# Kernel tuning notes

Hardware: AMD Instinct MI355X
Metric: run time of the kernel (lower is better)

Reference implementation:

```python
import jax, jax.numpy as jnp
import numpy as np

OS_FACTOR = 1.5

def setup_inputs() -> dict:
    key = jax.random.key(0)
    k = jax.random.split(key, 5)
    B, T, I, H = 64, 1024, 1024, 1024
    s = 1.0 / np.sqrt(H).astype(np.float32)
    return {
        "x": jax.random.normal(k[0], (B, T, I), dtype=jnp.float32),
        "W_ih": jax.random.normal(k[1], (H, I), dtype=jnp.float32) * s,
        "W_hh": jax.random.normal(k[2], (H, H), dtype=jnp.float32) * s,
        "b_ih": jax.random.normal(k[3], (H,), dtype=jnp.float32) * s,
        "b_hh": jax.random.normal(k[4], (H,), dtype=jnp.float32) * s,
    }

def reference(x, W_ih, W_hh, b_ih, b_hh):
    B, T, I = x.shape
    H = W_hh.shape[0]
    delay_near = int(np.floor(OS_FACTOR))   # 1
    delay_far = int(np.ceil(OS_FACTOR))     # 2
    alpha = jnp.float32(OS_FACTOR - delay_near)  # 0.5
    # Precompute input projection for all steps (same math, batched GEMM): [T,B,H]
    xw = jnp.einsum('bti,hi->tbh', x, W_ih) + b_ih + b_hh
    # Circular delay buffer of the last `delay_far` states, zero-initialized.
    # In the torch code, negative indices into the zero `states` buffer read zeros,
    # which matches a zero-initialized buffer here.
    buf0 = jnp.zeros((delay_far, B, H), dtype=x.dtype)

    def step(buf, xw_t):
        # buf[-1] = state at t-1, buf[0] = state at t-delay_far
        h_read = (1.0 - alpha) * buf[delay_far - delay_near] + alpha * buf[0]
        h = jnp.tanh(xw_t + h_read @ W_hh.T)
        buf = jnp.concatenate([buf[1:], h[None]], axis=0)
        return buf, h

    _, states = jax.lax.scan(step, buf0, xw)   # states: [T,B,H]
    states = jnp.swapaxes(states, 0, 1)        # [B,T,H]
    h_final = states[:, -1, :][None]           # [1,B,H]
    return states, h_final
```

## Files before the change

### kernel.cpp

```cpp
#include <hip/hip_runtime.h>
#include <stdint.h>
#include <stddef.h>

#define TT 1024
#define BB 64
#define HH 1024
#define II 1024

typedef __attribute__((ext_vector_type(8))) short s16x8;
typedef __attribute__((ext_vector_type(4))) float f32x4;

#define WS_FLAGS 512
#define WS_RING  4096

static __device__ __forceinline__ unsigned short f2bf(float f) {
    union { float f; unsigned int u; } v; v.f = f;
    return (unsigned short)((v.u + 0x7fffu + ((v.u >> 16) & 1u)) >> 16);
}

static __device__ __forceinline__ s16x8 pack8(float4 a, float4 b) {
    s16x8 v;
    v[0] = (short)f2bf(a.x); v[1] = (short)f2bf(a.y);
    v[2] = (short)f2bf(a.z); v[3] = (short)f2bf(a.w);
    v[4] = (short)f2bf(b.x); v[5] = (short)f2bf(b.y);
    v[6] = (short)f2bf(b.z); v[7] = (short)f2bf(b.w);
    return v;
}

static __device__ __forceinline__ f32x4 zero4() {
    f32x4 v = {0.f, 0.f, 0.f, 0.f};
    return v;
}

static __device__ __forceinline__ s16x8 ld16_sc01(const void* p) {
    s16x8 v;
    asm volatile("global_load_dwordx4 %0, %1, off sc0 sc1" : "=v"(v) : "v"(p));
    return v;
}
static __device__ __forceinline__ void st_h(void* p, unsigned short val) {
    unsigned v32 = val;
    asm volatile("global_store_short %0, %1, off sc0 sc1" :: "v"(p), "v"(v32) : "memory");
}
#define WAITV(n) do { asm volatile("s_waitcnt vmcnt(" #n ")" ::: "memory"); \
                      __builtin_amdgcn_sched_barrier(0); } while (0)

__global__ void init_ws(unsigned int* w) {
    for (int i = threadIdx.x; i < 640; i += 256)
        __hip_atomic_store(&w[i], 0u, __ATOMIC_RELAXED, __HIP_MEMORY_SCOPE_AGENT);
}

__global__ __launch_bounds__(256, 2) void xw_gemm(
    const float* __restrict__ X,
    const float* __restrict__ Wih,
    const float* __restrict__ bih,
    const float* __restrict__ bhh,
    float* __restrict__ out)
{
    __shared__ unsigned short As[128 * 64];
    __shared__ unsigned short Bs[128 * 64];

    const int tid  = threadIdx.x;
    const int lane = tid & 63;
    const int wid  = tid >> 6;
    const int bm = blockIdx.x >> 3;
    const int bn = blockIdx.x & 7;
    const size_t m0 = (size_t)bm * 128;
    const int n0 = bn * 128;
    const int wm = (wid >> 1) * 64;
    const int wn = (wid & 1) * 64;

    f32x4 acc[4][4];
#pragma unroll
    for (int i = 0; i < 4; ++i)
#pragma unroll
        for (int jj = 0; jj < 4; ++jj) acc[i][jj] = zero4();

    const int srow  = tid >> 1;
    const int shalf = tid & 1;
    const float* xp = X   + (m0 + srow) * (size_t)II + shalf * 32;
    const float* wp = Wih + (size_t)(n0 + srow) * II + shalf * 32;

    for (int kt = 0; kt < II / 64; ++kt) {
#pragma unroll
        for (int i = 0; i < 4; ++i) {
            float4 a0 = *(const float4*)(xp + i * 8);
            float4 a1 = *(const float4*)(xp + i * 8 + 4);
            float4 b0 = *(const float4*)(wp + i * 8);
            float4 b1 = *(const float4*)(wp + i * 8 + 4);
            const int c = shalf * 4 + i;
            const int cw = (c ^ (srow & 7)) << 3;
            *(s16x8*)&As[srow * 64 + cw] = pack8(a0, a1);
            *(s16x8*)&Bs[srow * 64 + cw] = pack8(b0, b1);
        }
        __syncthreads();

#pragma unroll
        for (int kk = 0; kk < 2; ++kk) {
            s16x8 af[4], bf[4];
            const int cs = kk * 4 + (lane >> 4);
#pragma unroll
            for (int mi = 0; mi < 4; ++mi) {
                const int r = wm + mi * 16 + (lane & 15);
                af[mi] = *(const s16x8*)&As[r * 64 + ((cs ^ (r & 7)) << 3)];
            }
#pragma unroll
            for (int ni = 0; ni < 4; ++ni) {
                const int r = wn + ni * 16 + (lane & 15);
                bf[ni] = *(const s16x8*)&Bs[r * 64 + ((cs ^ (r & 7)) << 3)];
            }
#pragma unroll
            for (int mi = 0; mi < 4; ++mi)
#pragma unroll
                for (int ni = 0; ni < 4; ++ni)
                    acc[mi][ni] = __builtin_amdgcn_mfma_f32_16x16x32_bf16(
                        af[mi], bf[ni], acc[mi][ni], 0, 0, 0);
        }
        __syncthreads();
        xp += 64; wp += 64;
    }

#pragma unroll
    for (int ni = 0; ni < 4; ++ni) {
        const int col = n0 + wn + ni * 16 + (lane & 15);
        const float bias = bih[col] + bhh[col];
#pragma unroll
        for (int mi = 0; mi < 4; ++mi) {
            const size_t row = m0 + wm + mi * 16 + ((lane >> 4) << 2);
#pragma unroll
            for (int r = 0; r < 4; ++r)
                out[(row + r) * (size_t)HH + col] = acc[mi][ni][r] + bias;
        }
    }
}

__global__ __launch_bounds__(256, 1) void rnn_scan(
    const float* __restrict__ Whh,
    float* __restrict__ out,
    void* __restrict__ ws)
{
    __shared__ unsigned short Hl[16 * 1024];

    const int tid  = threadIdx.x;
    const int lane = tid & 63;
    const int wid  = tid >> 6;
    const int g  = blockIdx.x >> 4;
    const int sl = blockIdx.x & 15;

    const int j  = sl * 64 + wid * 16 + (lane & 15);
    const int kg = lane >> 4;

    s16x8 bfr[32];
    {
        const float* wr = Whh + (size_t)j * HH + kg * 8;
#pragma unroll
        for (int c = 0; c < 32; ++c) {
            float4 p0 = *(const float4*)(wr + c * 32);
            float4 p1 = *(const float4*)(wr + c * 32 + 4);
            bfr[c] = pack8(p0, p1);
        }
    }

    unsigned* fl = (unsigned*)((char*)ws + WS_FLAGS) + g * 64;
    char* rg = (char*)ws + WS_RING + (size_t)g * 65536;

    const int srow = tid >> 4;
    const int sseg = tid & 15;
    const char* sbase0 = rg + srow * 2048 + sseg * 16;
    const char* sbase1 = sbase0 + 32768;

    const int arow = lane & 15;
    const int brow = kg * 4;
    float hprev[4];

#pragma unroll
    for (int r = 0; r < 4; ++r) {
        const int b = g * 16 + brow + r;
        const size_t idx = ((size_t)b * TT) * HH + j;
        const float h = tanhf(out[idx]);
        out[idx] = h;
        hprev[r] = h;
        st_h(rg + 32768 + (brow + r) * 2048 + j * 2, f2bf(0.5f * h));
    }
    asm volatile("s_waitcnt vmcnt(0)" ::: "memory");
    __syncthreads();
    if (tid == 0)
        __hip_atomic_store(&fl[sl], 1u, __ATOMIC_RELAXED, __HIP_MEMORY_SCOPE_AGENT);

#pragma unroll 1
    for (int t = 1; t < TT; ++t) {
        float xwv[4]; size_t xidx[4];
#pragma unroll
        for (int r = 0; r < 4; ++r) {
            const int b = g * 16 + brow + r;
            xidx[r] = ((size_t)b * TT + t) * HH + j;
            xwv[r] = out[xidx[r]];
        }

        {
            const unsigned* myp = fl + (lane & 15);
            for (;;) {
                unsigned v = __hip_atomic_load(myp, __ATOMIC_RELAXED,
                                               __HIP_MEMORY_SCOPE_AGENT);
                if (__all((int)(v >= (unsigned)t))) break;
                __builtin_amdgcn_s_sleep(1);
            }
            asm volatile("" ::: "memory");
            __builtin_amdgcn_sched_barrier(0);
        }

        {
            const char* sp = (t & 1) ? sbase1 : sbase0;
            s16x8 v[8];
#pragma unroll
            for (int i = 0; i < 8; ++i) v[i] = ld16_sc01(sp + i * 256);
#pragma unroll
            for (int i = 0; i < 8; ++i) {
                if (i == 0)      { WAITV(7); }
                else if (i == 1) { WAITV(6); }
                else if (i == 2) { WAITV(5); }
                else if (i == 3) { WAITV(4); }
                else if (i == 4) { WAITV(3); }
                else if (i == 5) { WAITV(2); }
                else if (i == 6) { WAITV(1); }
                else             { WAITV(0); }
                const int c = sseg + i * 16;
                *(s16x8*)&Hl[srow * 1024 + ((c ^ (srow & 7)) << 3)] = v[i];
            }
        }
        __syncthreads();

        f32x4 acc[4];
#pragma unroll
        for (int i = 0; i < 4; ++i) acc[i] = zero4();
#pragma unroll
        for (int kb = 0; kb < 4; ++kb) {
            s16x8 a8[8];
#pragma unroll
            for (int ki = 0; ki < 8; ++ki) {
                const int cs = (kb * 8 + ki) * 4 + kg;
                a8[ki] = *(const s16x8*)&Hl[arow * 1024 + ((cs ^ (arow & 7)) << 3)];
            }
#pragma unroll
            for (int ki = 0; ki < 8; ++ki)
                acc[ki & 3] = __builtin_amdgcn_mfma_f32_16x16x32_bf16(
                    a8[ki], bfr[kb * 8 + ki], acc[ki & 3], 0, 0, 0);
        }
        f32x4 accT = acc[0] + acc[1] + acc[2] + acc[3];

        char* rw = rg + (size_t)((t + 1) & 1) * 32768;
#pragma unroll
        for (int r = 0; r < 4; ++r) {
            const float h = tanhf(accT[r] + xwv[r]);
            out[xidx[r]] = h;
            if (t == TT - 1)
                out[(size_t)BB * TT * HH +
                    (size_t)(g * 16 + brow + r) * HH + j] = h;
            else
                st_h(rw + (brow + r) * 2048 + j * 2, f2bf(0.5f * (h + hprev[r])));
            hprev[r] = h;
        }
        if (t < TT - 1) {
            asm volatile("s_waitcnt vmcnt(0)" ::: "memory");
            __syncthreads();
            if (tid == 0)
                __hip_atomic_store(&fl[sl], (unsigned)(t + 1),
                                   __ATOMIC_RELAXED, __HIP_MEMORY_SCOPE_AGENT);
        }
    }
}

extern "C" void kernel_launch(void* const* d_in, const int* in_sizes, int n_in,
                              void* d_out, int out_size, void* d_ws, size_t ws_size,
                              hipStream_t stream)
{
    const float* X   = (const float*)d_in[0];
    const float* Wih = (const float*)d_in[1];
    const float* Whh = (const float*)d_in[2];
    const float* bih = (const float*)d_in[3];
    const float* bhh = (const float*)d_in[4];
    float* out = (float*)d_out;

    init_ws<<<dim3(1), dim3(256), 0, stream>>>((unsigned int*)d_ws);
    xw_gemm<<<dim3(4096), dim3(256), 0, stream>>>(X, Wih, bih, bhh, out);
    rnn_scan<<<dim3(64), dim3(256), 0, stream>>>(Whh, out, d_ws);
}
```

Measured before the change: 3.811 ms.

## Halve scan blocks, transpose MFMA operands, and vectorize state stores

The recurrent scan now runs 32 blocks of 512 threads, 8 per batch group instead of 16, so each block owns 128 hidden units and waits on fewer peer flags. W_hh becomes the A operand of the MFMA so each lane's output holds 4 contiguous hidden units for one batch row. That allows float4 loads and stores of xw and h, and 8-byte packed bf16 ring stores in place of scalar shorts. Flag polling moves to a single wave that reads all 8 flags with two vector loads, followed by a block barrier. In exchange each block does more work per step and runs a larger barrier, and only 32 CUs are used.

Measured after the change: 4.488 ms. 17.8% more time.

```diff
diff --git a/kernel.cpp b/kernel.cpp
--- a/kernel.cpp
+++ b/kernel.cpp
@@ -9,6 +9,8 @@
 
 typedef __attribute__((ext_vector_type(8))) short s16x8;
 typedef __attribute__((ext_vector_type(4))) float f32x4;
+typedef __attribute__((ext_vector_type(4))) unsigned u32x4;
+typedef __attribute__((ext_vector_type(2))) unsigned u32x2;
 
 #define WS_FLAGS 512
 #define WS_RING  4096
@@ -37,9 +39,14 @@
     asm volatile("global_load_dwordx4 %0, %1, off sc0 sc1" : "=v"(v) : "v"(p));
     return v;
 }
-static __device__ __forceinline__ void st_h(void* p, unsigned short val) {
-    unsigned v32 = val;
-    asm volatile("global_store_short %0, %1, off sc0 sc1" :: "v"(p), "v"(v32) : "memory");
+static __device__ __forceinline__ u32x4 ld16u_wait(const void* p) {
+    u32x4 v;
+    asm volatile("global_load_dwordx4 %0, %1, off sc0 sc1\n\ts_waitcnt vmcnt(0)"
+                 : "=v"(v) : "v"(p) : "memory");
+    return v;
+}
+static __device__ __forceinline__ void st8_sc01(void* p, u32x2 v) {
+    asm volatile("global_store_dwordx2 %0, %1, off sc0 sc1" :: "v"(p), "v"(v) : "memory");
 }
 #define WAITV(n) do { asm volatile("s_waitcnt vmcnt(" #n ")" ::: "memory"); \
                       __builtin_amdgcn_sched_barrier(0); } while (0)
@@ -133,7 +140,7 @@
     }
 }
 
-__global__ __launch_bounds__(256, 1) void rnn_scan(
+__global__ __launch_bounds__(512, 1) void rnn_scan(
     const float* __restrict__ Whh,
     float* __restrict__ out,
     void* __restrict__ ws)
@@ -143,43 +150,51 @@
     const int tid  = threadIdx.x;
     const int lane = tid & 63;
     const int wid  = tid >> 6;
-    const int g  = blockIdx.x >> 4;
-    const int sl = blockIdx.x & 15;
-
-    const int j  = sl * 64 + wid * 16 + (lane & 15);
+    const int g  = blockIdx.x >> 3;
+    const int sl = blockIdx.x & 7;
+
+    const int jb = sl * 128 + wid * 16;
     const int kg = lane >> 4;
 
-    s16x8 bfr[32];
+    s16x8 afr[32];
     {
-        const float* wr = Whh + (size_t)j * HH + kg * 8;
+        const float* wr = Whh + (size_t)(jb + (lane & 15)) * HH + kg * 8;
 #pragma unroll
         for (int c = 0; c < 32; ++c) {
             float4 p0 = *(const float4*)(wr + c * 32);
             float4 p1 = *(const float4*)(wr + c * 32 + 4);
-            bfr[c] = pack8(p0, p1);
+            afr[c] = pack8(p0, p1);
         }
     }
 
     unsigned* fl = (unsigned*)((char*)ws + WS_FLAGS) + g * 64;
     char* rg = (char*)ws + WS_RING + (size_t)g * 65536;
 
-    const int srow = tid >> 4;
-    const int sseg = tid & 15;
+    const int srow = tid >> 5;
+    const int sseg = tid & 31;
     const char* sbase0 = rg + srow * 2048 + sseg * 16;
     const char* sbase1 = sbase0 + 32768;
 
-    const int arow = lane & 15;
-    const int brow = kg * 4;
+    const int bl = lane & 15;
+    const int b  = g * 16 + bl;
+    const int f0 = jb + kg * 4;
+    const int hrow = bl;
+
     float hprev[4];
 
-#pragma unroll
-    for (int r = 0; r < 4; ++r) {
-        const int b = g * 16 + brow + r;
-        const size_t idx = ((size_t)b * TT) * HH + j;
-        const float h = tanhf(out[idx]);
-        out[idx] = h;
-        hprev[r] = h;
-        st_h(rg + 32768 + (brow + r) * 2048 + j * 2, f2bf(0.5f * h));
+    {
+        const size_t idx = ((size_t)b * TT) * HH + f0;
+        float4 xw4 = *(const float4*)(out + idx);
+        float4 st;
+        unsigned pk0, pk1;
+        st.x = tanhf(xw4.x); st.y = tanhf(xw4.y);
+        st.z = tanhf(xw4.z); st.w = tanhf(xw4.w);
+        hprev[0] = st.x; hprev[1] = st.y; hprev[2] = st.z; hprev[3] = st.w;
+        *(float4*)(out + idx) = st;
+        pk0 = (unsigned)f2bf(0.5f * st.x) | ((unsigned)f2bf(0.5f * st.y) << 16);
+        pk1 = (unsigned)f2bf(0.5f * st.z) | ((unsigned)f2bf(0.5f * st.w) << 16);
+        u32x2 pk; pk[0] = pk0; pk[1] = pk1;
+        st8_sc01(rg + 32768 + bl * 2048 + f0 * 2, pk);
     }
     asm volatile("s_waitcnt vmcnt(0)" ::: "memory");
     __syncthreads();
@@ -188,42 +203,35 @@
 
 #pragma unroll 1
     for (int t = 1; t < TT; ++t) {
-        float xwv[4]; size_t xidx[4];
-#pragma unroll
-        for (int r = 0; r < 4; ++r) {
-            const int b = g * 16 + brow + r;
-            xidx[r] = ((size_t)b * TT + t) * HH + j;
-            xwv[r] = out[xidx[r]];
-        }
-
-        {
-            const unsigned* myp = fl + (lane & 15);
+        const unsigned ut = (unsigned)t;
+
+        const size_t xidx = ((size_t)b * TT + t) * HH + f0;
+        float4 xw4 = *(const float4*)(out + xidx);
+
+        if (wid == 0) {
             for (;;) {
-                unsigned v = __hip_atomic_load(myp, __ATOMIC_RELAXED,
-                                               __HIP_MEMORY_SCOPE_AGENT);
-                if (__all((int)(v >= (unsigned)t))) break;
+                u32x4 a = ld16u_wait(fl);
+                u32x4 c = ld16u_wait(fl + 4);
+                if (a[0] >= ut && a[1] >= ut && a[2] >= ut && a[3] >= ut &&
+                    c[0] >= ut && c[1] >= ut && c[2] >= ut && c[3] >= ut) break;
                 __builtin_amdgcn_s_sleep(1);
             }
-            asm volatile("" ::: "memory");
-            __builtin_amdgcn_sched_barrier(0);
-        }
+        }
+        __syncthreads();
+        __builtin_amdgcn_sched_barrier(0);
 
         {
             const char* sp = (t & 1) ? sbase1 : sbase0;
-            s16x8 v[8];
-#pragma unroll
-            for (int i = 0; i < 8; ++i) v[i] = ld16_sc01(sp + i * 256);
-#pragma unroll
-            for (int i = 0; i < 8; ++i) {
-                if (i == 0)      { WAITV(7); }
-                else if (i == 1) { WAITV(6); }
-                else if (i == 2) { WAITV(5); }
-                else if (i == 3) { WAITV(4); }
-                else if (i == 4) { WAITV(3); }
-                else if (i == 5) { WAITV(2); }
-                else if (i == 6) { WAITV(1); }
+            s16x8 v[4];
+#pragma unroll
+            for (int i = 0; i < 4; ++i) v[i] = ld16_sc01(sp + i * 512);
+#pragma unroll
+            for (int i = 0; i < 4; ++i) {
+                if (i == 0)      { WAITV(3); }
+                else if (i == 1) { WAITV(2); }
+                else if (i == 2) { WAITV(1); }
                 else             { WAITV(0); }
-                const int c = sseg + i * 16;
+                const int c = sseg + i * 32;
                 *(s16x8*)&Hl[srow * 1024 + ((c ^ (srow & 7)) << 3)] = v[i];
             }
         }
@@ -234,30 +242,39 @@
         for (int i = 0; i < 4; ++i) acc[i] = zero4();
 #pragma unroll
         for (int kb = 0; kb < 4; ++kb) {
-            s16x8 a8[8];
+            s16x8 h8[8];
 #pragma unroll
             for (int ki = 0; ki < 8; ++ki) {
                 const int cs = (kb * 8 + ki) * 4 + kg;
-                a8[ki] = *(const s16x8*)&Hl[arow * 1024 + ((cs ^ (arow & 7)) << 3)];
+                h8[ki] = *(const s16x8*)&Hl[hrow * 1024 + ((cs ^ (hrow & 7)) << 3)];
             }
 #pragma unroll
             for (int ki = 0; ki < 8; ++ki)
                 acc[ki & 3] = __builtin_amdgcn_mfma_f32_16x16x32_bf16(
-                    a8[ki], bfr[kb * 8 + ki], acc[ki & 3], 0, 0, 0);
+                    afr[kb * 8 + ki], h8[ki], acc[ki & 3], 0, 0, 0);
         }
         f32x4 accT = acc[0] + acc[1] + acc[2] + acc[3];
 
-        char* rw = rg + (size_t)((t + 1) & 1) * 32768;
-#pragma unroll
-        for (int r = 0; r < 4; ++r) {
-            const float h = tanhf(accT[r] + xwv[r]);
-            out[xidx[r]] = h;
-            if (t == TT - 1)
-                out[(size_t)BB * TT * HH +
-                    (size_t)(g * 16 + brow + r) * HH + j] = h;
-            else
-                st_h(rw + (brow + r) * 2048 + j * 2, f2bf(0.5f * (h + hprev[r])));
-            hprev[r] = h;
+        {
+            float4 st;
+            float hn[4];
+#pragma unroll
+            for (int r = 0; r < 4; ++r) hn[r] = tanhf(accT[r] + ((const float*)&xw4)[r]);
+            st.x = hn[0]; st.y = hn[1]; st.z = hn[2]; st.w = hn[3];
+            *(float4*)(out + xidx) = st;
+            if (t == TT - 1) {
+                *(float4*)(out + (size_t)BB * TT * HH + (size_t)b * HH + f0) = st;
+            } else {
+                u32x2 pk;
+                pk[0] = (unsigned)f2bf(0.5f * (hn[0] + hprev[0])) |
+                        ((unsigned)f2bf(0.5f * (hn[1] + hprev[1])) << 16);
+                pk[1] = (unsigned)f2bf(0.5f * (hn[2] + hprev[2])) |
+                        ((unsigned)f2bf(0.5f * (hn[3] + hprev[3])) << 16);
+                char* rw = rg + (size_t)((t + 1) & 1) * 32768;
+                st8_sc01(rw + bl * 2048 + f0 * 2, pk);
+            }
+#pragma unroll
+            for (int r = 0; r < 4; ++r) hprev[r] = hn[r];
         }
         if (t < TT - 1) {
             asm volatile("s_waitcnt vmcnt(0)" ::: "memory");
@@ -282,5 +299,5 @@
 
     init_ws<<<dim3(1), dim3(256), 0, stream>>>((unsigned int*)d_ws);
     xw_gemm<<<dim3(4096), dim3(256), 0, stream>>>(X, Wih, bih, bhh, out);
-    rnn_scan<<<dim3(64), dim3(256), 0, stream>>>(Whh, out, d_ws);
-}
+    rnn_scan<<<dim3(32), dim3(512), 0, stream>>>(Whh, out, d_ws);
+}
```
